# Optimization experiments

Measured on AMD Instinct MI355X. Metric: run time of the kernel, lower is better.

## Reference

```python
import jax, jax.numpy as jnp
import numpy as np

H = 128   # LSTM hidden size
T = 120   # sequence length
F = 4     # input features


def setup_inputs() -> dict:
    key = jax.random.key(0)
    ks = jax.random.split(key, 11)
    B = 4096
    return {
        "x": jax.random.normal(ks[0], (B, T, F), dtype=jnp.float32),
        "h0": jax.random.uniform(ks[1], (B, H), dtype=jnp.float32),
        "c0": jax.random.uniform(ks[2], (B, H), dtype=jnp.float32),
        "W_ih": jax.random.normal(ks[3], (4 * H, F), dtype=jnp.float32) * 0.05,
        "W_hh": jax.random.normal(ks[4], (4 * H, H), dtype=jnp.float32) * 0.05,
        "b_ih": jax.random.normal(ks[5], (4 * H,), dtype=jnp.float32) * 0.05,
        "b_hh": jax.random.normal(ks[6], (4 * H,), dtype=jnp.float32) * 0.05,
        "fc1_w": jax.random.normal(ks[7], (100, T * H), dtype=jnp.float32) * 0.01,
        "fc1_b": jax.random.normal(ks[8], (100,), dtype=jnp.float32) * 0.01,
        "fc2_w": jax.random.normal(ks[9], (10, 100), dtype=jnp.float32) * 0.1,
        "fc2_b": jax.random.normal(ks[10], (10,), dtype=jnp.float32) * 0.1,
    }


def _lstm(x, h0, c0, W_ih, W_hh, b_ih, b_hh):
    # Precompute input-dependent part of the gates for all timesteps at once.
    # PyTorch gate order: i, f, g, o.  gates_x: [T, B, 4H]
    gates_x = jnp.einsum('btf,gf->tbg', x, W_ih) + b_ih + b_hh

    def step(carry, gx):
        h, c = carry
        g = gx + h @ W_hh.T                      # [B, 4H]
        i = jax.nn.sigmoid(g[:, 0 * H:1 * H])
        f = jax.nn.sigmoid(g[:, 1 * H:2 * H])
        gg = jnp.tanh(g[:, 2 * H:3 * H])
        o = jax.nn.sigmoid(g[:, 3 * H:4 * H])
        c = f * c + i * gg
        h = o * jnp.tanh(c)
        return (h, c), h

    (_, _), hs = jax.lax.scan(step, (h0, c0), gates_x)  # hs: [T, B, H]
    return hs


def reference(x, h0, c0, W_ih, W_hh, b_ih, b_hh, fc1_w, fc1_b, fc2_w, fc2_b):
    B = x.shape[0]
    hs = _lstm(x, h0, c0, W_ih, W_hh, b_ih, b_hh)        # [T, B, H]
    feat = hs.transpose(1, 0, 2).reshape(B, T * H)        # [B, T*H]
    hid = jax.nn.relu(feat @ fc1_w.T + fc1_b)             # [B, 100]
    logits = hid @ fc2_w.T + fc2_b                        # [B, 10]
    return jax.nn.log_softmax(logits, axis=-1)
```

## Files before the change

### kernel.cpp

```cpp
#include <hip/hip_runtime.h>

#define T_LEN 120
#define H 128
#define ROWS 16
#define FC1_STRIDE 15360

#define OFF_WHH   0u
#define OFF_WXB   131072u
#define OFF_FC1W  163840u
#define OFF_FC1B  4096000u

typedef short short8 __attribute__((ext_vector_type(8)));
typedef float f32x4 __attribute__((ext_vector_type(4)));
typedef float f32x2 __attribute__((ext_vector_type(2)));
typedef unsigned int ui32x4 __attribute__((ext_vector_type(4)));

#define L2E 1.4426950408889634f
#define SWZ(r) (((((r) & 7) ^ (((r) >> 3) << 1))) << 4)
#define MFMA __builtin_amdgcn_mfma_f32_16x16x32_bf16

__device__ __forceinline__ unsigned short f2bu(float f) {
  unsigned u = __builtin_bit_cast(unsigned, f);
  u += 0x7fffu + ((u >> 16) & 1u);
  return (unsigned short)(u >> 16);
}
__device__ __forceinline__ unsigned cvt_pk_bf16(float lo, float hi) {
  unsigned r;
  asm("v_cvt_pk_bf16_f32 %0, %1, %2" : "=v"(r) : "v"(lo), "v"(hi));
  return r;
}
__device__ __forceinline__ float gate_scale(int row) {
  return ((row >> 7) == 2) ? 2.0f * L2E : -L2E;
}

__global__ void prep_all(const float* __restrict__ W_ih, const float* __restrict__ W_hh,
                         const float* __restrict__ b_ih, const float* __restrict__ b_hh,
                         const float* __restrict__ fc1_w, const float* __restrict__ fc1_b,
                         unsigned char* __restrict__ ws) {
  if (blockIdx.x < 1024) {
    unsigned short* w = (unsigned short*)(ws + OFF_FC1W);
    int j = blockIdx.x >> 3;
    int c0 = ((blockIdx.x & 7) * 256 + threadIdx.x) * 8;
    if (c0 >= FC1_STRIDE) return;
    short8 v = {0, 0, 0, 0, 0, 0, 0, 0};
    if (j < 100) {
      const float* src = fc1_w + j * FC1_STRIDE + c0;
#pragma unroll
      for (int e = 0; e < 8; ++e) ((unsigned short*)&v)[e] = f2bu(src[e]);
    }
    *(short8*)(w + j * FC1_STRIDE + c0) = v;
  } else {
    unsigned short* whh = (unsigned short*)(ws + OFF_WHH);
    unsigned short* wxb = (unsigned short*)(ws + OFF_WXB);
    float* fb = (float*)(ws + OFF_FC1B);
    int tid = (blockIdx.x - 1024) * 256 + threadIdx.x;
    const int nt = 8 * 256;
    for (int i = tid; i < 512 * 128; i += nt) {
      int row = i >> 7;
      whh[i] = f2bu(W_hh[i] * gate_scale(row));
    }
    for (int i = tid; i < 512 * 32; i += nt) {
      int j = i >> 5, k = i & 31;
      float s = gate_scale(j);
      float v = 0.f;
      if (k < 4) v = W_ih[j * 4 + k] * s;
      else if (k == 4) v = (b_ih[j] + b_hh[j]) * s;
      wxb[i] = f2bu(v);
    }
    for (int i = tid; i < 128; i += nt) fb[i] = (i < 100) ? fc1_b[i] : 0.f;
  }
}

__global__ __launch_bounds__(512, 2)
void lstm_fused(const float* __restrict__ x, const float* __restrict__ h0,
                const float* __restrict__ c0, const float* __restrict__ fc2_w,
                const float* __restrict__ fc2_b, const unsigned char* __restrict__ ws,
                float* __restrict__ out) {
  __shared__ __align__(16) unsigned char xab[T_LEN * 256];
  __shared__ __align__(16) unsigned char h_lds[2 * 4096];
  __shared__ __align__(16) float fc2w_s[1000];
  __shared__ float fc2b_s[10];
  __shared__ float logit_s[ROWS * 12];

  const int tid = threadIdx.x;
  const int w = tid >> 6;
  const int l = tid & 63;
  const int lq = l >> 4;
  const int lc = l & 15;
  const int r0 = blockIdx.x * ROWS;
  const int hcol = w * 16 + lc;

  const unsigned short* Whh = (const unsigned short*)(ws + OFF_WHH);
  const unsigned short* Wxb = (const unsigned short*)(ws + OFF_WXB);
  const unsigned short* FC1 = (const unsigned short*)(ws + OFF_FC1W);
  const float* FC1B = (const float*)(ws + OFF_FC1B);

  for (int i = tid; i < 1000; i += 512) fc2w_s[i] = fc2_w[i];
  if (tid < 10) fc2b_s[tid] = fc2_b[tid];

  for (int i = tid; i < ROWS * T_LEN; i += 512) {
    int rr = i / T_LEN, t = i - rr * T_LEN;
    f32x4 xv = *(const f32x4*)(x + (r0 + rr) * (T_LEN * 4) + t * 4);
    unsigned w0 = cvt_pk_bf16(xv[0], xv[1]);
    unsigned w1 = cvt_pk_bf16(xv[2], xv[3]);
    ui32x4 pk = {w0, w1, 0x3f80u, 0u};
    *(ui32x4*)(xab + t * 256 + rr * 16) = pk;
  }
  for (int e = tid * 2; e < ROWS * H; e += 1024) {
    int r = e >> 7, c = e & 127;
    unsigned u = (unsigned)f2bu(h0[(r0 + r) * H + c]) |
                 ((unsigned)f2bu(h0[(r0 + r) * H + c + 1]) << 16);
    *(unsigned*)(h_lds + 4096 + r * 256 + ((2 * c) ^ SWZ(r))) = u;
  }
  float c_reg[4];
#pragma unroll
  for (int q = 0; q < 4; ++q) c_reg[q] = c0[(r0 + lq * 4 + q) * H + hcol];

  short8 bhh[4][4], bxb[4];
#pragma unroll
  for (int g = 0; g < 4; ++g) {
    int n0 = (g * 8 + w) * 16;
#pragma unroll
    for (int kk = 0; kk < 4; ++kk)
      bhh[g][kk] = *(const short8*)(Whh + (n0 + lc) * H + kk * 32 + lq * 8);
    bxb[g] = *(const short8*)(Wxb + (n0 + lc) * 32 + lq * 8);
  }
  const unsigned short* fc1row = FC1 + (w * 16 + lc) * FC1_STRIDE;
  f32x4 facc = {0.f, 0.f, 0.f, 0.f};

  unsigned soff[4];
#pragma unroll
  for (int q = 0; q < 4; ++q) {
    int r = lq * 4 + q;
    soff[q] = (unsigned)(r * 256 + ((2 * hcol) ^ SWZ(r)));
  }

  __syncthreads();

  short8 ha[4];
#pragma unroll
  for (int kk = 0; kk < 4; ++kk)
    ha[kk] = *(const short8*)(h_lds + 4096 + lc * 256 + ((kk * 64 + lq * 16) ^ SWZ(lc)));
  short8 xa = *(const short8*)(xab + lc * 16);

  const f32x4 zero4 = {0.f, 0.f, 0.f, 0.f};
  f32x4 accX0 = MFMA(xa, bxb[0], zero4, 0, 0, 0);
  f32x4 accX1 = MFMA(xa, bxb[1], zero4, 0, 0, 0);
  f32x4 accX2 = MFMA(xa, bxb[2], zero4, 0, 0, 0);
  f32x4 accX3 = MFMA(xa, bxb[3], zero4, 0, 0, 0);

  short8 fbh0 = {0,0,0,0,0,0,0,0}, fbh1 = {0,0,0,0,0,0,0,0};
  short8 fbh2 = {0,0,0,0,0,0,0,0}, fbh3 = {0,0,0,0,0,0,0,0};

  const f32x2 one2 = {1.f, 1.f};

#pragma unroll 2
  for (int t = 0; t < T_LEN; ++t) {
    const unsigned short* fp = fc1row + t * 128 + lq * 8;
    short8 nfb0 = *(const short8*)(fp + 0);
    short8 nfb1 = *(const short8*)(fp + 32);
    short8 nfb2 = *(const short8*)(fp + 64);
    short8 nfb3 = *(const short8*)(fp + 96);

    __builtin_amdgcn_s_setprio(1);
    f32x4 lo0 = accX0, lo1 = accX1, lo2 = accX2, lo3 = accX3;
    f32x4 hi0 = zero4, hi1 = zero4, hi2 = zero4, hi3 = zero4;
    lo0 = MFMA(ha[0], bhh[0][0], lo0, 0, 0, 0);
    lo1 = MFMA(ha[0], bhh[1][0], lo1, 0, 0, 0);
    lo2 = MFMA(ha[0], bhh[2][0], lo2, 0, 0, 0);
    lo3 = MFMA(ha[0], bhh[3][0], lo3, 0, 0, 0);
    hi0 = MFMA(ha[2], bhh[0][2], hi0, 0, 0, 0);
    hi1 = MFMA(ha[2], bhh[1][2], hi1, 0, 0, 0);
    hi2 = MFMA(ha[2], bhh[2][2], hi2, 0, 0, 0);
    hi3 = MFMA(ha[2], bhh[3][2], hi3, 0, 0, 0);
    lo0 = MFMA(ha[1], bhh[0][1], lo0, 0, 0, 0);
    lo1 = MFMA(ha[1], bhh[1][1], lo1, 0, 0, 0);
    lo2 = MFMA(ha[1], bhh[2][1], lo2, 0, 0, 0);
    lo3 = MFMA(ha[1], bhh[3][1], lo3, 0, 0, 0);
    hi0 = MFMA(ha[3], bhh[0][3], hi0, 0, 0, 0);
    hi1 = MFMA(ha[3], bhh[1][3], hi1, 0, 0, 0);
    hi2 = MFMA(ha[3], bhh[2][3], hi2, 0, 0, 0);
    hi3 = MFMA(ha[3], bhh[3][3], hi3, 0, 0, 0);

    facc = MFMA(ha[0], fbh0, facc, 0, 0, 0);
    facc = MFMA(ha[1], fbh1, facc, 0, 0, 0);
    facc = MFMA(ha[2], fbh2, facc, 0, 0, 0);
    facc = MFMA(ha[3], fbh3, facc, 0, 0, 0);

    f32x4 acc0 = lo0 + hi0;
    f32x4 acc1 = lo1 + hi1;
    f32x4 acc2 = lo2 + hi2;
    f32x4 acc3 = lo3 + hi3;

    fbh0 = nfb0; fbh1 = nfb1; fbh2 = nfb2; fbh3 = nfb3;
    int tn = (t + 1 < T_LEN) ? t + 1 : t;
    short8 xan = *(const short8*)(xab + tn * 256 + lc * 16);

    unsigned char* hw = h_lds + (t & 1) * 4096;
#pragma unroll
    for (int qp = 0; qp < 2; ++qp) {
      const int q0 = qp * 2, q1 = q0 + 1;
      f32x2 ea = {__builtin_amdgcn_exp2f(acc0[q0]), __builtin_amdgcn_exp2f(acc0[q1])};
      f32x2 eb = {__builtin_amdgcn_exp2f(acc1[q0]), __builtin_amdgcn_exp2f(acc1[q1])};
      f32x2 ec = {__builtin_amdgcn_exp2f(acc2[q0]), __builtin_amdgcn_exp2f(acc2[q1])};
      f32x2 ed = {__builtin_amdgcn_exp2f(acc3[q0]), __builtin_amdgcn_exp2f(acc3[q1])};
      f32x2 a = ea + one2, b = eb + one2, d = ec + one2, e = ed + one2;
      f32x2 ab = a * b, de = d * e;
      float rAB = __builtin_amdgcn_rcpf(ab[0] * ab[1]);
      float rDE = __builtin_amdgcn_rcpf(de[0] * de[1]);
      f32x2 rab = {rAB * ab[1], rAB * ab[0]};
      f32x2 rde = {rDE * de[1], rDE * de[0]};
      f32x2 iv = b * rab, fv = a * rab;
      f32x2 erde = e * rde;
      f32x2 gv = one2 - (erde + erde);
      f32x2 ov = d * rde;
      f32x2 cp = {c_reg[q0], c_reg[q1]};
      f32x2 cn = fv * cp + iv * gv;
      c_reg[q0] = cn[0]; c_reg[q1] = cn[1];
      f32x2 cs = cn * 2.8853900817779268f;
      f32x2 et = {__builtin_amdgcn_exp2f(cs[0]), __builtin_amdgcn_exp2f(cs[1])};
      f32x2 tt = et + one2;
      float rT = __builtin_amdgcn_rcpf(tt[0] * tt[1]);
      float hv0 = ov[0] * (1.f - 2.f * (rT * tt[1]));
      float hv1 = ov[1] * (1.f - 2.f * (rT * tt[0]));
      unsigned pk = cvt_pk_bf16(hv0, hv1);
      *(unsigned short*)(hw + soff[q0]) = (unsigned short)pk;
      *(unsigned short*)(hw + soff[q1]) = (unsigned short)(pk >> 16);
    }
    __builtin_amdgcn_s_setprio(0);

    asm volatile("s_waitcnt lgkmcnt(0)" ::: "memory");
    __builtin_amdgcn_s_barrier();
    asm volatile("" ::: "memory");

#pragma unroll
    for (int kk = 0; kk < 4; ++kk)
      ha[kk] = *(const short8*)(hw + lc * 256 + ((kk * 64 + lq * 16) ^ SWZ(lc)));
    accX0 = MFMA(xan, bxb[0], zero4, 0, 0, 0);
    accX1 = MFMA(xan, bxb[1], zero4, 0, 0, 0);
    accX2 = MFMA(xan, bxb[2], zero4, 0, 0, 0);
    accX3 = MFMA(xan, bxb[3], zero4, 0, 0, 0);
  }
  facc = MFMA(ha[0], fbh0, facc, 0, 0, 0);
  facc = MFMA(ha[1], fbh1, facc, 0, 0, 0);
  facc = MFMA(ha[2], fbh2, facc, 0, 0, 0);
  facc = MFMA(ha[3], fbh3, facc, 0, 0, 0);

  float bias = FC1B[hcol];
  __syncthreads();
  float* hid = (float*)xab;
#pragma unroll
  for (int q = 0; q < 4; ++q) {
    float v = facc[q] + bias;
    hid[(lq * 4 + q) * 132 + hcol] = v > 0.f ? v : 0.f;
  }
  __syncthreads();
  if (tid < 160) {
    int r = tid & 15, k = tid >> 4;
    float a = fc2b_s[k];
#pragma unroll 4
    for (int j = 0; j < 100; ++j) a += hid[r * 132 + j] * fc2w_s[k * 100 + j];
    logit_s[r * 12 + k] = a;
  }
  __syncthreads();
  if (tid < 16) {
    int r = tid;
    float m = logit_s[r * 12];
#pragma unroll
    for (int k = 1; k < 10; ++k) m = fmaxf(m, logit_s[r * 12 + k]);
    float s = 0.f;
#pragma unroll
    for (int k = 0; k < 10; ++k)
      s += __builtin_amdgcn_exp2f(L2E * (logit_s[r * 12 + k] - m));
    float ls = __builtin_amdgcn_logf(s) * 0.6931471805599453f;
#pragma unroll
    for (int k = 0; k < 10; ++k)
      out[(r0 + r) * 10 + k] = logit_s[r * 12 + k] - m - ls;
  }
}

extern "C" void kernel_launch(void* const* d_in, const int* in_sizes, int n_in,
                              void* d_out, int out_size, void* d_ws, size_t ws_size,
                              hipStream_t stream) {
  const float* x     = (const float*)d_in[0];
  const float* h0    = (const float*)d_in[1];
  const float* c0    = (const float*)d_in[2];
  const float* W_ih  = (const float*)d_in[3];
  const float* W_hh  = (const float*)d_in[4];
  const float* b_ih  = (const float*)d_in[5];
  const float* b_hh  = (const float*)d_in[6];
  const float* fc1_w = (const float*)d_in[7];
  const float* fc1_b = (const float*)d_in[8];
  const float* fc2_w = (const float*)d_in[9];
  const float* fc2_b = (const float*)d_in[10];
  float* out = (float*)d_out;
  unsigned char* ws = (unsigned char*)d_ws;

  prep_all<<<1032, 256, 0, stream>>>(W_ih, W_hh, b_ih, b_hh, fc1_w, fc1_b, ws);
  lstm_fused<<<256, 512, 0, stream>>>(x, h0, c0, fc2_w, fc2_b, ws, out);
}
```

Baseline: 136.1 us.

## Split batch into 8-row blocks of 4 waves and batch FC1 over an 8-step h ring

Each block now handles 8 batch rows with 256 threads (4 waves, each owning 32 hidden columns) instead of 16 rows with 512 threads, doubling the grid to 512 blocks. The 8 valid rows are spread across the padded 16-row MFMA tile, with the unused rows zeroed. Hidden states are kept in an 8-slot LDS ring, and the FC1 accumulation is deferred and done in bursts every 8 timesteps, taking it off the per-step critical path. The aim is more blocks to fill the CUs and a shorter recurrence step. The cost is half-empty MFMA tiles, twice the recurrent MFMA count per row, and an extra barrier every 8 steps.

```diff
diff --git a/kernel.cpp b/kernel.cpp
--- a/kernel.cpp
+++ b/kernel.cpp
@@ -2,7 +2,6 @@
 
 #define T_LEN 120
 #define H 128
-#define ROWS 16
 #define FC1_STRIDE 15360
 
 #define OFF_WHH   0u
@@ -71,139 +70,136 @@
   }
 }
 
-__global__ __launch_bounds__(512, 2)
+__global__ __launch_bounds__(256, 2)
 void lstm_fused(const float* __restrict__ x, const float* __restrict__ h0,
                 const float* __restrict__ c0, const float* __restrict__ fc2_w,
                 const float* __restrict__ fc2_b, const unsigned char* __restrict__ ws,
                 float* __restrict__ out) {
-  __shared__ __align__(16) unsigned char xab[T_LEN * 256];
-  __shared__ __align__(16) unsigned char h_lds[2 * 4096];
+  __shared__ __align__(16) unsigned char xab[T_LEN * 128];
+  __shared__ __align__(16) unsigned char hring[8 * 4096];
   __shared__ __align__(16) float fc2w_s[1000];
   __shared__ float fc2b_s[10];
-  __shared__ float logit_s[ROWS * 12];
+  __shared__ float logit_s[8 * 12];
 
   const int tid = threadIdx.x;
   const int w = tid >> 6;
   const int l = tid & 63;
   const int lq = l >> 4;
   const int lc = l & 15;
-  const int r0 = blockIdx.x * ROWS;
-  const int hcol = w * 16 + lc;
+  const int r0 = blockIdx.x * 8;
 
   const unsigned short* Whh = (const unsigned short*)(ws + OFF_WHH);
   const unsigned short* Wxb = (const unsigned short*)(ws + OFF_WXB);
   const unsigned short* FC1 = (const unsigned short*)(ws + OFF_FC1W);
   const float* FC1B = (const float*)(ws + OFF_FC1B);
 
-  for (int i = tid; i < 1000; i += 512) fc2w_s[i] = fc2_w[i];
+  for (int i = tid; i < 1000; i += 256) fc2w_s[i] = fc2_w[i];
   if (tid < 10) fc2b_s[tid] = fc2_b[tid];
 
-  for (int i = tid; i < ROWS * T_LEN; i += 512) {
-    int rr = i / T_LEN, t = i - rr * T_LEN;
-    f32x4 xv = *(const f32x4*)(x + (r0 + rr) * (T_LEN * 4) + t * 4);
+  for (int i = tid; i < 8 * T_LEN; i += 256) {
+    int j = i / T_LEN, t = i - j * T_LEN;
+    f32x4 xv = *(const f32x4*)(x + (r0 + j) * (T_LEN * 4) + t * 4);
     unsigned w0 = cvt_pk_bf16(xv[0], xv[1]);
     unsigned w1 = cvt_pk_bf16(xv[2], xv[3]);
     ui32x4 pk = {w0, w1, 0x3f80u, 0u};
-    *(ui32x4*)(xab + t * 256 + rr * 16) = pk;
-  }
-  for (int e = tid * 2; e < ROWS * H; e += 1024) {
-    int r = e >> 7, c = e & 127;
-    unsigned u = (unsigned)f2bu(h0[(r0 + r) * H + c]) |
-                 ((unsigned)f2bu(h0[(r0 + r) * H + c + 1]) << 16);
-    *(unsigned*)(h_lds + 4096 + r * 256 + ((2 * c) ^ SWZ(r))) = u;
-  }
-  float c_reg[4];
-#pragma unroll
-  for (int q = 0; q < 4; ++q) c_reg[q] = c0[(r0 + lq * 4 + q) * H + hcol];
-
-  short8 bhh[4][4], bxb[4];
-#pragma unroll
-  for (int g = 0; g < 4; ++g) {
-    int n0 = (g * 8 + w) * 16;
-#pragma unroll
-    for (int kk = 0; kk < 4; ++kk)
-      bhh[g][kk] = *(const short8*)(Whh + (n0 + lc) * H + kk * 32 + lq * 8);
-    bxb[g] = *(const short8*)(Wxb + (n0 + lc) * 32 + lq * 8);
-  }
-  const unsigned short* fc1row = FC1 + (w * 16 + lc) * FC1_STRIDE;
-  f32x4 facc = {0.f, 0.f, 0.f, 0.f};
-
-  unsigned soff[4];
-#pragma unroll
-  for (int q = 0; q < 4; ++q) {
-    int r = lq * 4 + q;
-    soff[q] = (unsigned)(r * 256 + ((2 * hcol) ^ SWZ(r)));
-  }
+    *(ui32x4*)(xab + t * 128 + j * 16) = pk;
+  }
+  for (int i = tid; i < 4096; i += 256) {
+    int slot = i >> 9;
+    int rem = i & 511;
+    int dr = rem >> 6;
+    int word = rem & 63;
+    int tr = ((dr >> 1) << 2) + 2 + (dr & 1);
+    *(unsigned*)(hring + slot * 4096 + tr * 256 + word * 4) = 0u;
+  }
+  for (int i = tid; i < 512; i += 256) {
+    int e = i * 2;
+    int j = e >> 7, c = e & 127;
+    int tr = ((j >> 1) << 2) + (j & 1);
+    const float* hp = h0 + (r0 + j) * H + c;
+    unsigned u = (unsigned)f2bu(hp[0]) | ((unsigned)f2bu(hp[1]) << 16);
+    *(unsigned*)(hring + 7 * 4096 + tr * 256 + ((2 * c) ^ SWZ(tr))) = u;
+  }
+  float c_reg[2][2];
+#pragma unroll
+  for (int c = 0; c < 2; ++c)
+#pragma unroll
+    for (int q = 0; q < 2; ++q)
+      c_reg[c][q] = c0[(r0 + lq * 2 + q) * H + w * 32 + c * 16 + lc];
+
+  short8 bhh[4][2][4], bxb[4][2];
+#pragma unroll
+  for (int g = 0; g < 4; ++g)
+#pragma unroll
+    for (int c = 0; c < 2; ++c) {
+      int n0 = g * 128 + w * 32 + c * 16;
+#pragma unroll
+      for (int kk = 0; kk < 4; ++kk)
+        bhh[g][c][kk] = *(const short8*)(Whh + (n0 + lc) * H + kk * 32 + lq * 8);
+      bxb[g][c] = *(const short8*)(Wxb + (n0 + lc) * 32 + lq * 8);
+    }
+  f32x4 facc0 = {0.f, 0.f, 0.f, 0.f}, facc1 = {0.f, 0.f, 0.f, 0.f};
+
+  unsigned soff[2][2];
+#pragma unroll
+  for (int c = 0; c < 2; ++c)
+#pragma unroll
+    for (int q = 0; q < 2; ++q) {
+      int r = lq * 4 + q;
+      int col = w * 32 + c * 16 + lc;
+      soff[c][q] = (unsigned)(r * 256 + ((2 * col) ^ SWZ(r)));
+    }
+
+  const int jr = ((lc >> 2) << 1) | (lc & 1);
 
   __syncthreads();
 
   short8 ha[4];
 #pragma unroll
   for (int kk = 0; kk < 4; ++kk)
-    ha[kk] = *(const short8*)(h_lds + 4096 + lc * 256 + ((kk * 64 + lq * 16) ^ SWZ(lc)));
-  short8 xa = *(const short8*)(xab + lc * 16);
+    ha[kk] = *(const short8*)(hring + 7 * 4096 + lc * 256 + ((kk * 64 + lq * 16) ^ SWZ(lc)));
+  short8 xa = *(const short8*)(xab + jr * 16);
 
   const f32x4 zero4 = {0.f, 0.f, 0.f, 0.f};
-  f32x4 accX0 = MFMA(xa, bxb[0], zero4, 0, 0, 0);
-  f32x4 accX1 = MFMA(xa, bxb[1], zero4, 0, 0, 0);
-  f32x4 accX2 = MFMA(xa, bxb[2], zero4, 0, 0, 0);
-  f32x4 accX3 = MFMA(xa, bxb[3], zero4, 0, 0, 0);
-
-  short8 fbh0 = {0,0,0,0,0,0,0,0}, fbh1 = {0,0,0,0,0,0,0,0};
-  short8 fbh2 = {0,0,0,0,0,0,0,0}, fbh3 = {0,0,0,0,0,0,0,0};
-
   const f32x2 one2 = {1.f, 1.f};
 
-#pragma unroll 2
   for (int t = 0; t < T_LEN; ++t) {
-    const unsigned short* fp = fc1row + t * 128 + lq * 8;
-    short8 nfb0 = *(const short8*)(fp + 0);
-    short8 nfb1 = *(const short8*)(fp + 32);
-    short8 nfb2 = *(const short8*)(fp + 64);
-    short8 nfb3 = *(const short8*)(fp + 96);
+    unsigned char* hw = hring + ((t & 7) << 12);
 
     __builtin_amdgcn_s_setprio(1);
-    f32x4 lo0 = accX0, lo1 = accX1, lo2 = accX2, lo3 = accX3;
-    f32x4 hi0 = zero4, hi1 = zero4, hi2 = zero4, hi3 = zero4;
-    lo0 = MFMA(ha[0], bhh[0][0], lo0, 0, 0, 0);
-    lo1 = MFMA(ha[0], bhh[1][0], lo1, 0, 0, 0);
-    lo2 = MFMA(ha[0], bhh[2][0], lo2, 0, 0, 0);
-    lo3 = MFMA(ha[0], bhh[3][0], lo3, 0, 0, 0);
-    hi0 = MFMA(ha[2], bhh[0][2], hi0, 0, 0, 0);
-    hi1 = MFMA(ha[2], bhh[1][2], hi1, 0, 0, 0);
-    hi2 = MFMA(ha[2], bhh[2][2], hi2, 0, 0, 0);
-    hi3 = MFMA(ha[2], bhh[3][2], hi3, 0, 0, 0);
-    lo0 = MFMA(ha[1], bhh[0][1], lo0, 0, 0, 0);
-    lo1 = MFMA(ha[1], bhh[1][1], lo1, 0, 0, 0);
-    lo2 = MFMA(ha[1], bhh[2][1], lo2, 0, 0, 0);
-    lo3 = MFMA(ha[1], bhh[3][1], lo3, 0, 0, 0);
-    hi0 = MFMA(ha[3], bhh[0][3], hi0, 0, 0, 0);
-    hi1 = MFMA(ha[3], bhh[1][3], hi1, 0, 0, 0);
-    hi2 = MFMA(ha[3], bhh[2][3], hi2, 0, 0, 0);
-    hi3 = MFMA(ha[3], bhh[3][3], hi3, 0, 0, 0);
-
-    facc = MFMA(ha[0], fbh0, facc, 0, 0, 0);
-    facc = MFMA(ha[1], fbh1, facc, 0, 0, 0);
-    facc = MFMA(ha[2], fbh2, facc, 0, 0, 0);
-    facc = MFMA(ha[3], fbh3, facc, 0, 0, 0);
-
-    f32x4 acc0 = lo0 + hi0;
-    f32x4 acc1 = lo1 + hi1;
-    f32x4 acc2 = lo2 + hi2;
-    f32x4 acc3 = lo3 + hi3;
-
-    fbh0 = nfb0; fbh1 = nfb1; fbh2 = nfb2; fbh3 = nfb3;
+    f32x4 a00 = MFMA(xa, bxb[0][0], zero4, 0, 0, 0);
+    f32x4 a01 = MFMA(xa, bxb[1][0], zero4, 0, 0, 0);
+    f32x4 a02 = MFMA(xa, bxb[2][0], zero4, 0, 0, 0);
+    f32x4 a03 = MFMA(xa, bxb[3][0], zero4, 0, 0, 0);
+    f32x4 a10 = MFMA(xa, bxb[0][1], zero4, 0, 0, 0);
+    f32x4 a11 = MFMA(xa, bxb[1][1], zero4, 0, 0, 0);
+    f32x4 a12 = MFMA(xa, bxb[2][1], zero4, 0, 0, 0);
+    f32x4 a13 = MFMA(xa, bxb[3][1], zero4, 0, 0, 0);
+#pragma unroll
+    for (int kk = 0; kk < 4; ++kk) {
+      a00 = MFMA(ha[kk], bhh[0][0][kk], a00, 0, 0, 0);
+      a01 = MFMA(ha[kk], bhh[1][0][kk], a01, 0, 0, 0);
+      a02 = MFMA(ha[kk], bhh[2][0][kk], a02, 0, 0, 0);
+      a03 = MFMA(ha[kk], bhh[3][0][kk], a03, 0, 0, 0);
+      a10 = MFMA(ha[kk], bhh[0][1][kk], a10, 0, 0, 0);
+      a11 = MFMA(ha[kk], bhh[1][1][kk], a11, 0, 0, 0);
+      a12 = MFMA(ha[kk], bhh[2][1][kk], a12, 0, 0, 0);
+      a13 = MFMA(ha[kk], bhh[3][1][kk], a13, 0, 0, 0);
+    }
+
     int tn = (t + 1 < T_LEN) ? t + 1 : t;
-    short8 xan = *(const short8*)(xab + tn * 256 + lc * 16);
-
-    unsigned char* hw = h_lds + (t & 1) * 4096;
-#pragma unroll
-    for (int qp = 0; qp < 2; ++qp) {
-      const int q0 = qp * 2, q1 = q0 + 1;
-      f32x2 ea = {__builtin_amdgcn_exp2f(acc0[q0]), __builtin_amdgcn_exp2f(acc0[q1])};
-      f32x2 eb = {__builtin_amdgcn_exp2f(acc1[q0]), __builtin_amdgcn_exp2f(acc1[q1])};
-      f32x2 ec = {__builtin_amdgcn_exp2f(acc2[q0]), __builtin_amdgcn_exp2f(acc2[q1])};
-      f32x2 ed = {__builtin_amdgcn_exp2f(acc3[q0]), __builtin_amdgcn_exp2f(acc3[q1])};
+    short8 xan = *(const short8*)(xab + tn * 128 + jr * 16);
+
+#pragma unroll
+    for (int c = 0; c < 2; ++c) {
+      f32x4 gi = c ? a10 : a00;
+      f32x4 gf = c ? a11 : a01;
+      f32x4 gg = c ? a12 : a02;
+      f32x4 go = c ? a13 : a03;
+      f32x2 ea = {__builtin_amdgcn_exp2f(gi[0]), __builtin_amdgcn_exp2f(gi[1])};
+      f32x2 eb = {__builtin_amdgcn_exp2f(gf[0]), __builtin_amdgcn_exp2f(gf[1])};
+      f32x2 ec = {__builtin_amdgcn_exp2f(gg[0]), __builtin_amdgcn_exp2f(gg[1])};
+      f32x2 ed = {__builtin_amdgcn_exp2f(go[0]), __builtin_amdgcn_exp2f(go[1])};
       f32x2 a = ea + one2, b = eb + one2, d = ec + one2, e = ed + one2;
       f32x2 ab = a * b, de = d * e;
       float rAB = __builtin_amdgcn_rcpf(ab[0] * ab[1]);
@@ -214,9 +210,9 @@
       f32x2 erde = e * rde;
       f32x2 gv = one2 - (erde + erde);
       f32x2 ov = d * rde;
-      f32x2 cp = {c_reg[q0], c_reg[q1]};
+      f32x2 cp = {c_reg[c][0], c_reg[c][1]};
       f32x2 cn = fv * cp + iv * gv;
-      c_reg[q0] = cn[0]; c_reg[q1] = cn[1];
+      c_reg[c][0] = cn[0]; c_reg[c][1] = cn[1];
       f32x2 cs = cn * 2.8853900817779268f;
       f32x2 et = {__builtin_amdgcn_exp2f(cs[0]), __builtin_amdgcn_exp2f(cs[1])};
       f32x2 tt = et + one2;
@@ -224,8 +220,8 @@
       float hv0 = ov[0] * (1.f - 2.f * (rT * tt[1]));
       float hv1 = ov[1] * (1.f - 2.f * (rT * tt[0]));
       unsigned pk = cvt_pk_bf16(hv0, hv1);
-      *(unsigned short*)(hw + soff[q0]) = (unsigned short)pk;
-      *(unsigned short*)(hw + soff[q1]) = (unsigned short)(pk >> 16);
+      *(unsigned short*)(hw + soff[c][0]) = (unsigned short)pk;
+      *(unsigned short*)(hw + soff[c][1]) = (unsigned short)(pk >> 16);
     }
     __builtin_amdgcn_s_setprio(0);
 
@@ -236,34 +232,56 @@
 #pragma unroll
     for (int kk = 0; kk < 4; ++kk)
       ha[kk] = *(const short8*)(hw + lc * 256 + ((kk * 64 + lq * 16) ^ SWZ(lc)));
-    accX0 = MFMA(xan, bxb[0], zero4, 0, 0, 0);
-    accX1 = MFMA(xan, bxb[1], zero4, 0, 0, 0);
-    accX2 = MFMA(xan, bxb[2], zero4, 0, 0, 0);
-    accX3 = MFMA(xan, bxb[3], zero4, 0, 0, 0);
-  }
-  facc = MFMA(ha[0], fbh0, facc, 0, 0, 0);
-  facc = MFMA(ha[1], fbh1, facc, 0, 0, 0);
-  facc = MFMA(ha[2], fbh2, facc, 0, 0, 0);
-  facc = MFMA(ha[3], fbh3, facc, 0, 0, 0);
-
-  float bias = FC1B[hcol];
+    xa = xan;
+
+    if ((t & 7) == 7) {
+      int tb = t - 7;
+      const unsigned short* f0base = FC1 + (w * 32 + lc) * FC1_STRIDE + lq * 8;
+      const unsigned short* f1base = FC1 + (w * 32 + 16 + lc) * FC1_STRIDE + lq * 8;
+#pragma unroll 2
+      for (int s = 0; s < 8; ++s) {
+        const unsigned short* f0 = f0base + (tb + s) * 128;
+        const unsigned short* f1 = f1base + (tb + s) * 128;
+        short8 fb0[4], fb1[4], hs[4];
+#pragma unroll
+        for (int kk = 0; kk < 4; ++kk) {
+          fb0[kk] = *(const short8*)(f0 + kk * 32);
+          fb1[kk] = *(const short8*)(f1 + kk * 32);
+          hs[kk] = *(const short8*)(hring + s * 4096 + lc * 256 + ((kk * 64 + lq * 16) ^ SWZ(lc)));
+        }
+#pragma unroll
+        for (int kk = 0; kk < 4; ++kk) {
+          facc0 = MFMA(hs[kk], fb0[kk], facc0, 0, 0, 0);
+          facc1 = MFMA(hs[kk], fb1[kk], facc1, 0, 0, 0);
+        }
+      }
+      asm volatile("s_waitcnt lgkmcnt(0)" ::: "memory");
+      __builtin_amdgcn_s_barrier();
+      asm volatile("" ::: "memory");
+    }
+  }
+
+  float bias0 = FC1B[w * 32 + lc];
+  float bias1 = FC1B[w * 32 + 16 + lc];
   __syncthreads();
   float* hid = (float*)xab;
 #pragma unroll
-  for (int q = 0; q < 4; ++q) {
-    float v = facc[q] + bias;
-    hid[(lq * 4 + q) * 132 + hcol] = v > 0.f ? v : 0.f;
+  for (int q = 0; q < 2; ++q) {
+    float v0 = facc0[q] + bias0;
+    float v1 = facc1[q] + bias1;
+    hid[(lq * 2 + q) * 132 + w * 32 + lc] = v0 > 0.f ? v0 : 0.f;
+    hid[(lq * 2 + q) * 132 + w * 32 + 16 + lc] = v1 > 0.f ? v1 : 0.f;
   }
   __syncthreads();
-  if (tid < 160) {
-    int r = tid & 15, k = tid >> 4;
+  if (tid < 80) {
+    int r = tid & 7, k = tid >> 3;
     float a = fc2b_s[k];
 #pragma unroll 4
     for (int j = 0; j < 100; ++j) a += hid[r * 132 + j] * fc2w_s[k * 100 + j];
     logit_s[r * 12 + k] = a;
   }
   __syncthreads();
-  if (tid < 16) {
+  if (tid < 8) {
     int r = tid;
     float m = logit_s[r * 12];
 #pragma unroll
@@ -297,5 +315,5 @@
   unsigned char* ws = (unsigned char*)d_ws;
 
   prep_all<<<1032, 256, 0, stream>>>(W_ih, W_hh, b_ih, b_hh, fc1_w, fc1_b, ws);
-  lstm_fused<<<256, 512, 0, stream>>>(x, h0, c0, fc2_w, fc2_b, ws, out);
-}
+  lstm_fused<<<512, 256, 0, stream>>>(x, h0, c0, fc2_w, fc2_b, ws, out);
+}
```

Result: slower. 369.1 us (+171.2%).
